# Kernel optimization log

Hardware: AMD Instinct MI355X
Metric: run time of the kernel (lower is better)

Reference implementation:

```python
import jax, jax.numpy as jnp
import numpy as np

Z_LOSS_COEF = 0.001
TOP_K = 8


def setup_inputs() -> dict:
    key = jax.random.key(0)
    ks = jax.random.split(key, 8)
    D, L, E, F, FS = 1024, 256, 64, 256, 1024  # d_model, latent, experts, latent d_ff, shared d_ff
    B, S = 1, 1024
    x = jax.random.normal(ks[0], (B, S, D), jnp.float32)
    gate_w = jax.random.normal(ks[1], (E, D), jnp.float32) * 0.01  # router, std=0.01 init
    expert_bias = jnp.zeros((E,), jnp.float32)  # load-balancing bias buffer
    down_w = jax.random.normal(ks[2], (L, D), jnp.float32) * 0.02
    up_w = jax.random.normal(ks[3], (D, L), jnp.float32) * 0.02
    shared_gu_w = jax.random.normal(ks[4], (2 * FS, D), jnp.float32) * 0.02
    shared_down_w = jax.random.normal(ks[5], (D, FS), jnp.float32) * 0.02
    exp_gu_w = jax.random.normal(ks[6], (E, L, 2 * F), jnp.float32) * 0.02  # [E,K,N] layout
    exp_down_w = jax.random.normal(ks[7], (E, F, L), jnp.float32) * 0.02
    return {"x": x, "gate_w": gate_w, "expert_bias": expert_bias,
            "down_w": down_w, "up_w": up_w,
            "shared_gu_w": shared_gu_w, "shared_down_w": shared_down_w,
            "exp_gu_w": exp_gu_w, "exp_down_w": exp_down_w}


def reference(x, gate_w, expert_bias, down_w, up_w, shared_gu_w, shared_down_w, exp_gu_w, exp_down_w):
    B, S, D = x.shape
    xf = x.reshape(-1, D)                     # [N, D]
    N = xf.shape[0]
    E = gate_w.shape[0]
    # ---- AuxLossFreeRouter (full d_model input) ----
    logits = xf @ gate_w.T                    # [N, E]
    z_loss = Z_LOSS_COEF * jnp.mean(jax.nn.logsumexp(logits, axis=-1) ** 2)
    affinity = jax.nn.sigmoid(logits)
    scores = affinity + expert_bias           # bias only affects selection, not weights
    _, sel = jax.lax.top_k(scores, TOP_K)     # [N, K] int32
    sel_aff = jnp.take_along_axis(affinity, sel, axis=1)
    gw = sel_aff / (sel_aff.sum(-1, keepdims=True) + 1e-9)  # [N, K]
    # sparse combine matrix [N, E]
    combine = jnp.zeros((N, E), xf.dtype).at[jnp.arange(N)[:, None], sel].add(gw)
    # ---- shared SwiGLU expert at full d_model ----
    sh = xf @ shared_gu_w.T
    g, u = jnp.split(sh, 2, axis=-1)
    shared_out = (jax.nn.silu(g) * u) @ shared_down_w.T     # [N, D]
    # ---- latent batched experts: down-project, dense-over-E SwiGLU, sparse combine ----
    lat = xf @ down_w.T                       # [N, L]
    h = jnp.einsum('nl,elf->nef', lat, exp_gu_w)            # [N, E, 2F]
    hg, hu = jnp.split(h, 2, axis=-1)
    hid = jax.nn.silu(hg) * hu                # [N, E, F]
    y = jnp.einsum('nef,efl->nel', hid, exp_down_w)         # [N, E, L]
    routed_lat = jnp.einsum('ne,nel->nl', combine, y)       # sparse top-k combine
    routed = routed_lat @ up_w.T              # [N, D]
    out = (shared_out + routed).reshape(B, S, D)
    return out, z_loss
```

## Files before the change

### kernel.cpp

```cpp
#include <hip/hip_runtime.h>
#include <stdint.h>


using f32x4 = __attribute__((ext_vector_type(4))) float;
using s16x8 = __attribute__((ext_vector_type(8))) short;

#define MFMA_BF16(a, b, c) __builtin_amdgcn_mfma_f32_16x16x32_bf16((a), (b), (c), 0, 0, 0)
#define AS1 __attribute__((address_space(1)))
#define AS3 __attribute__((address_space(3)))

__device__ __forceinline__ unsigned short f2bf(float f) {
  union { float f; uint32_t u; } v; v.f = f;
  uint32_t u = v.u;
  u += 0x7FFFu + ((u >> 16) & 1u);
  return (unsigned short)(u >> 16);
}
__device__ __forceinline__ float bf2f(unsigned short h) {
  union { uint32_t u; float f; } v; v.u = ((uint32_t)h) << 16;
  return v.f;
}
__device__ __forceinline__ float silu_f(float x) { return x / (1.f + expf(-x)); }

__device__ __forceinline__ size_t TIDX(int row, int col, int K) {
  return (((size_t)((row >> 7) * (K >> 5) + (col >> 5))) << 12) +
         (size_t)((((col >> 3) & 3) << 10) + ((row & 127) << 3) + (col & 7));
}

struct Args {
  const float *x, *gate, *down, *sgu, *sdw, *up, *egu, *edw, *bias;
  unsigned short *xb, *Wcat, *Bf, *egut, *edwt, *Abuf, *lat_g, *hide, *ybuf;
  float *C1, *Pf, *out;
  int *counts, *slot_nk;
  float *gw_nk;
};

__global__ void pack_kernel(Args a) {
  __shared__ union { float lin[128 * 33]; float tp[32][33]; } sm;
  const int b = blockIdx.x, t = threadIdx.x;
  if (b == 0) {
    if (t < 64) a.counts[t] = 0;
    if (t == 64) a.out[1048576] = 0.f;
  }
  if (b < 1184) {
    int rt, kt, K;
    const float* base = nullptr;
    unsigned short* dst;
    if (b < 608)      { rt = b >> 5;          kt = b & 31; K = 1024; dst = a.Wcat; }
    else if (b < 928) { int q = b - 608; rt = q / 40; kt = q % 40; K = 1280; dst = a.Bf; }
    else              { int q = b - 928; rt = q >> 5; kt = q & 31; K = 1024; dst = a.xb; base = a.x; }

    const int r = t >> 1, half = t & 1;
    const int gr = rt * 128 + r;
    const int c0 = kt * 32 + half * 16;
    const float* s;
    if (b < 608) {
      if (gr < 64)       s = a.gate + (size_t)gr * 1024 + c0;
      else if (gr < 320) s = a.down + (size_t)(gr - 64) * 1024 + c0;
      else if (gr < 384) s = nullptr;
      else {
        const int i = gr - 384;
        s = a.sgu + (size_t)((i >> 1) + (i & 1) * 1024) * 1024 + c0;
      }
    } else if (b < 928) {
      s = (c0 < 1024) ? a.sdw + (size_t)gr * 1024 + c0
                      : a.up + (size_t)gr * 256 + (c0 - 1024);
    } else {
      s = base + (size_t)gr * 1024 + c0;
    }
#pragma unroll
    for (int i = 0; i < 4; ++i) {
      float4 v = s ? *(const float4*)(s + i * 4) : make_float4(0.f, 0.f, 0.f, 0.f);
      sm.lin[r * 33 + half * 16 + i * 4 + 0] = v.x;
      sm.lin[r * 33 + half * 16 + i * 4 + 1] = v.y;
      sm.lin[r * 33 + half * 16 + i * 4 + 2] = v.z;
      sm.lin[r * 33 + half * 16 + i * 4 + 3] = v.w;
    }
    __syncthreads();
    const int j = t >> 6, r0 = (t & 63) * 2;
    unsigned short tmp[16];
#pragma unroll
    for (int rr = 0; rr < 2; ++rr)
#pragma unroll
      for (int c = 0; c < 8; ++c)
        tmp[rr * 8 + c] = f2bf(sm.lin[(r0 + rr) * 33 + j * 8 + c]);
    unsigned short* d = dst + ((size_t)(rt * (K >> 5) + kt) << 12) + t * 16;
    *(s16x8*)d = *(s16x8*)tmp;
    *(s16x8*)(d + 8) = *(s16x8*)(tmp + 8);
  } else {
    const float* src; unsigned short* dst; int lds, tr, tc; bool inter;
    if (b < 9376) {
      const int q = b - 1184, e = q >> 7, tt = q & 127;
      tr = tt >> 4; tc = tt & 15; lds = 512; inter = true;
      src = a.egu + (size_t)e * 131072; dst = a.egut + (size_t)e * 131072;
    } else {
      const int q = b - 9376, e = q >> 6, tt = q & 63;
      tr = tt >> 3; tc = tt & 7; lds = 256; inter = false;
      src = a.edw + (size_t)e * 65536; dst = a.edwt + (size_t)e * 65536;
    }
    const int r = t >> 3, c4 = (t & 7) * 4;
    float4 v = *(const float4*)(src + (size_t)(tr * 32 + r) * lds + tc * 32 + c4);
    sm.tp[r][c4 + 0] = v.x; sm.tp[r][c4 + 1] = v.y;
    sm.tp[r][c4 + 2] = v.z; sm.tp[r][c4 + 3] = v.w;
    __syncthreads();
    const int n = tc * 32 + r;
    const int orow = inter ? ((n < 256) ? 2 * n : 2 * (n - 256) + 1) : n;
    const int col = tr * 32 + c4;
    ushort4 o = make_ushort4(f2bf(sm.tp[c4 + 0][r]), f2bf(sm.tp[c4 + 1][r]),
                             f2bf(sm.tp[c4 + 2][r]), f2bf(sm.tp[c4 + 3][r]));
    *(ushort4*)(dst + TIDX(orow, col, 256)) = o;
  }
}

template <int MODE>
__device__ void wgemm64(const unsigned short* __restrict__ A, int KA, int m0,
                        const unsigned short* __restrict__ B, int KB, int n0,
                        int kt0, int nkt, void* __restrict__ out, int ld, int coff,
                        unsigned short* __restrict__ L) {
  const int lane = threadIdx.x & 63;
  const unsigned short* Abase =
      A + (((size_t)((m0 >> 7) * (KA >> 5) + kt0)) << 12) + ((m0 >> 6) & 1) * 512;
  const unsigned short* Bbase =
      B + (((size_t)((n0 >> 7) * (KB >> 5) + kt0)) << 12) + ((n0 >> 6) & 1) * 512;
  unsigned short* As = L;
  unsigned short* Bs = L + 4096;

  auto stage = [&](int kt, int buf) {
    const unsigned short* at = Abase + ((size_t)kt << 12);
    const unsigned short* bt = Bbase + ((size_t)kt << 12);
#pragma unroll
    for (int j = 0; j < 4; ++j)
      __builtin_amdgcn_global_load_lds((const AS1 void*)(at + j * 1024 + lane * 8),
                                       (AS3 void*)(As + buf * 2048 + j * 512), 16, 0, 0);
#pragma unroll
    for (int j = 0; j < 4; ++j)
      __builtin_amdgcn_global_load_lds((const AS1 void*)(bt + j * 1024 + lane * 8),
                                       (AS3 void*)(Bs + buf * 2048 + j * 512), 16, 0, 0);
  };

  f32x4 acc[4][4] = {};
  stage(0, 0);
  const int kh = lane >> 4, r16 = lane & 15;
  for (int kt = 0; kt < nkt; ++kt) {
    if (kt + 1 < nkt) {
      stage(kt + 1, (kt + 1) & 1);
      asm volatile("s_waitcnt vmcnt(8)" ::: "memory");
    } else {
      asm volatile("s_waitcnt vmcnt(0)" ::: "memory");
    }
    const unsigned short* Ac = As + (kt & 1) * 2048;
    const unsigned short* Bc = Bs + (kt & 1) * 2048;
    s16x8 af[4], bfr[4];
#pragma unroll
    for (int m = 0; m < 4; ++m)
      af[m] = *(const s16x8*)(Ac + kh * 512 + (m * 16 + r16) * 8);
#pragma unroll
    for (int n = 0; n < 4; ++n)
      bfr[n] = *(const s16x8*)(Bc + kh * 512 + (n * 16 + r16) * 8);
#pragma unroll
    for (int m = 0; m < 4; ++m)
#pragma unroll
      for (int n = 0; n < 4; ++n)
        acc[m][n] = MFMA_BF16(af[m], bfr[n], acc[m][n]);
  }

#pragma unroll
  for (int m = 0; m < 4; ++m) {
    const int rb = m0 + m * 16 + (lane >> 4) * 4;
#pragma unroll
    for (int n = 0; n < 4; ++n) {
      const int c = n0 + n * 16 + (lane & 15);
      if (MODE == 0) {
        float* O = (float*)out;
#pragma unroll
        for (int j = 0; j < 4; ++j) O[(size_t)(rb + j) * ld + c] = acc[m][n][j];
      } else if (MODE == 1) {
        unsigned short* O = (unsigned short*)out;
#pragma unroll
        for (int j = 0; j < 4; ++j) O[TIDX(rb + j, c, ld)] = f2bf(acc[m][n][j]);
      } else {
        unsigned short* O = (unsigned short*)out;
        const int col = (c - coff) >> 1;
#pragma unroll
        for (int j = 0; j < 4; ++j) {
          const float v = acc[m][n][j];
          const float u = __shfl_xor(v, 1);
          if (!(lane & 1)) O[TIDX(rb + j, col, ld)] = f2bf(silu_f(v) * u);
        }
      }
    }
  }
}

__global__ __launch_bounds__(64, 3) void wg1(const unsigned short* __restrict__ xb,
                                             const unsigned short* __restrict__ Wcat,
                                             float* __restrict__ C1,
                                             unsigned short* __restrict__ Abuf) {
  __shared__ __align__(16) unsigned short L[8192];
  const int b = blockIdx.x, mt = b / 38, nt = b % 38;
  if (nt < 6)
    wgemm64<0>(xb, 1024, mt * 64, Wcat, 1024, nt * 64, 0, 32, C1, 384, 0, L);
  else
    wgemm64<2>(xb, 1024, mt * 64, Wcat, 1024, nt * 64, 0, 32, Abuf, 1280, 384, L);
}

__global__ __launch_bounds__(64, 3) void wgGU(const unsigned short* __restrict__ lat_g,
                                              const unsigned short* __restrict__ egut,
                                              unsigned short* __restrict__ hide,
                                              const int* __restrict__ counts) {
  __shared__ __align__(16) unsigned short L[8192];
  const int b = blockIdx.x, e = b >> 5, rt = (b >> 3) & 3, ct = b & 7;
  int cnt = counts[e];
  if (cnt > 256) cnt = 256;
  if (rt * 64 >= cnt) return;
  wgemm64<2>(lat_g, 256, e * 256 + rt * 64, egut + (size_t)e * 131072, 256,
             ct * 64, 0, 8, hide, 256, 0, L);
}

__global__ __launch_bounds__(64, 3) void wgDW(const unsigned short* __restrict__ hide,
                                              const unsigned short* __restrict__ edwt,
                                              unsigned short* __restrict__ ybuf,
                                              const int* __restrict__ counts) {
  __shared__ __align__(16) unsigned short L[8192];
  const int b = blockIdx.x, e = b >> 4, rt = (b >> 2) & 3, ct = b & 3;
  int cnt = counts[e];
  if (cnt > 256) cnt = 256;
  if (rt * 64 >= cnt) return;
  wgemm64<1>(hide, 256, e * 256 + rt * 64, edwt + (size_t)e * 65536, 256,
             ct * 64, 0, 8, ybuf, 256, 0, L);
}

__global__ __launch_bounds__(64, 3) void wgF(const unsigned short* __restrict__ Abuf,
                                             const unsigned short* __restrict__ Bf,
                                             float* __restrict__ Pf) {
  __shared__ __align__(16) unsigned short L[8192];
  const int b = blockIdx.x, kc = b >> 8, mt = (b >> 4) & 15, nt = b & 15;
  wgemm64<0>(Abuf, 1280, mt * 64, Bf, 1280, nt * 64, kc * 10, 10,
             Pf + (size_t)kc * 1048576, 1024, 0, L);
}

__global__ void addF(const float* __restrict__ Pf, float* __restrict__ out) {
  const size_t i = (size_t)blockIdx.x * 1024 + threadIdx.x * 4;
  float4 s = *(const float4*)(Pf + i);
  const float4 b1 = *(const float4*)(Pf + 1048576 + i);
  const float4 b2 = *(const float4*)(Pf + 2097152 + i);
  const float4 b3 = *(const float4*)(Pf + 3145728 + i);
  s.x += b1.x + b2.x + b3.x; s.y += b1.y + b2.y + b3.y;
  s.z += b1.z + b2.z + b3.z; s.w += b1.w + b2.w + b3.w;
  *(float4*)(out + i) = s;
}

__global__ void router_kernel(Args a) {
  const int n = blockIdx.x * 4 + (threadIdx.x >> 6);
  const int lane = threadIdx.x & 63;
  const float* row = a.C1 + (size_t)n * 384;
  const float logit = row[lane];

  float mx = logit;
#pragma unroll
  for (int d = 32; d; d >>= 1) mx = fmaxf(mx, __shfl_xor(mx, d));
  float se = expf(logit - mx);
#pragma unroll
  for (int d = 32; d; d >>= 1) se += __shfl_xor(se, d);
  if (lane == 0) {
    const float lse = mx + logf(se);
    atomicAdd(a.out + 1048576, 0.001f * lse * lse * (1.f / 1024.f));
  }

  const float aff = 1.f / (1.f + expf(-logit));
  float s = aff + a.bias[lane];

  float asum = 0.f;
  int e_mine = 0; float a_mine = 0.f;
#pragma unroll
  for (int k = 0; k < 8; ++k) {
    float m2 = s;
#pragma unroll
    for (int d = 32; d; d >>= 1) m2 = fmaxf(m2, __shfl_xor(m2, d));
    const unsigned long long blt = __ballot(s == m2);
    const int idx = __ffsll(blt) - 1;
    const float af_ = __shfl(aff, idx);
    asum += af_;
    if (lane == k) { e_mine = idx; a_mine = af_; }
    if (lane == idx) s = -3.0e38f;
  }
  const float inv = 1.f / (asum + 1e-9f);

  int slot = 0;
  if (lane < 8) {
    int pos = atomicAdd(&a.counts[e_mine], 1);
    if (pos > 255) pos = 255;
    slot = e_mine * 256 + pos;
    a.slot_nk[(size_t)n * 8 + lane] = slot;
    a.gw_nk[(size_t)n * 8 + lane] = a_mine * inv;
  }

  const float4 lv = *(const float4*)(row + 64 + lane * 4);
  const ushort4 lb = make_ushort4(f2bf(lv.x), f2bf(lv.y), f2bf(lv.z), f2bf(lv.w));
#pragma unroll
  for (int k = 0; k < 8; ++k) {
    const int sl = __shfl(slot, k);
    *(ushort4*)(a.lat_g + TIDX(sl, lane * 4, 256)) = lb;
  }
}

__global__ void combine_kernel(Args a) {
  const int n = blockIdx.x * 4 + (threadIdx.x >> 6);
  const int l4 = (threadIdx.x & 63) * 4;
  float a0 = 0.f, a1 = 0.f, a2 = 0.f, a3 = 0.f;
#pragma unroll
  for (int k = 0; k < 8; ++k) {
    const int sl = a.slot_nk[(size_t)n * 8 + k];
    const float g = a.gw_nk[(size_t)n * 8 + k];
    const ushort4 yv = *(const ushort4*)(a.ybuf + TIDX(sl, l4, 256));
    a0 += g * bf2f(yv.x); a1 += g * bf2f(yv.y);
    a2 += g * bf2f(yv.z); a3 += g * bf2f(yv.w);
  }
  *(ushort4*)(a.Abuf + TIDX(n, 1024 + l4, 1280)) =
      make_ushort4(f2bf(a0), f2bf(a1), f2bf(a2), f2bf(a3));
}

extern "C" void kernel_launch(void* const* d_in, const int* in_sizes, int n_in,
                              void* d_out, int out_size, void* d_ws, size_t ws_size,
                              hipStream_t stream) {
  (void)in_sizes; (void)n_in; (void)out_size; (void)ws_size;
  Args a;
  a.x    = (const float*)d_in[0];
  a.gate = (const float*)d_in[1];
  a.bias = (const float*)d_in[2];
  a.down = (const float*)d_in[3];
  a.up   = (const float*)d_in[4];
  a.sgu  = (const float*)d_in[5];
  a.sdw  = (const float*)d_in[6];
  a.egu  = (const float*)d_in[7];
  a.edw  = (const float*)d_in[8];
  a.out  = (float*)d_out;

  char* w = (char*)d_ws;
  auto alloc = [&](size_t bytes) { char* p = w; w += (bytes + 255) & ~(size_t)255; return p; };
  a.xb    = (unsigned short*)alloc(1048576ull * 2);
  a.Wcat  = (unsigned short*)alloc(2432ull * 1024 * 2);
  a.Bf    = (unsigned short*)alloc(1024ull * 1280 * 2);
  a.egut  = (unsigned short*)alloc(64ull * 512 * 256 * 2);
  a.edwt  = (unsigned short*)alloc(64ull * 256 * 256 * 2);
  a.C1    = (float*)alloc(1024ull * 384 * 4);
  a.Abuf  = (unsigned short*)alloc(1024ull * 1280 * 2);
  a.lat_g = (unsigned short*)alloc(16384ull * 256 * 2);
  a.hide  = (unsigned short*)alloc(16384ull * 256 * 2);
  a.ybuf  = (unsigned short*)alloc(16384ull * 256 * 2);
  a.Pf    = (float*)alloc(4ull * 1048576 * 4);
  a.counts  = (int*)alloc(64 * 4);
  a.slot_nk = (int*)alloc(8192 * 4);
  a.gw_nk   = (float*)alloc(8192 * 4);

  pack_kernel<<<dim3(13472), dim3(256), 0, stream>>>(a);
  wg1<<<dim3(608), dim3(64), 0, stream>>>(a.xb, a.Wcat, a.C1, a.Abuf);
  router_kernel<<<dim3(256), dim3(256), 0, stream>>>(a);
  wgGU<<<dim3(2048), dim3(64), 0, stream>>>(a.lat_g, a.egut, a.hide, a.counts);
  wgDW<<<dim3(1024), dim3(64), 0, stream>>>(a.hide, a.edwt, a.ybuf, a.counts);
  combine_kernel<<<dim3(256), dim3(256), 0, stream>>>(a);
  wgF<<<dim3(1024), dim3(64), 0, stream>>>(a.Abuf, a.Bf, a.Pf);
  addF<<<dim3(1024), dim3(256), 0, stream>>>(a.Pf, a.out);
}
```

Measured before the change: 126.6 us.

## Load GEMM fragments directly from global into registers, dropping LDS staging

The single-wave 64x64 GEMM tile no longer stages A and B through LDS with global_load_lds. Each lane now loads its MFMA fragments straight from the pre-tiled global layout into registers, double-buffered two k-steps ahead. This removes the LDS round trip and the shared-memory allocation, which may raise occupancy. In exchange it uses more registers and relies on the tiled layout giving coalesced 16-byte loads, with latency hidden only by the register prefetch.

```diff
diff --git a/kernel.cpp b/kernel.cpp
--- a/kernel.cpp
+++ b/kernel.cpp
@@ -6,8 +6,6 @@
 using s16x8 = __attribute__((ext_vector_type(8))) short;
 
 #define MFMA_BF16(a, b, c) __builtin_amdgcn_mfma_f32_16x16x32_bf16((a), (b), (c), 0, 0, 0)
-#define AS1 __attribute__((address_space(1)))
-#define AS3 __attribute__((address_space(3)))
 
 __device__ __forceinline__ unsigned short f2bf(float f) {
   union { float f; uint32_t u; } v; v.f = f;
@@ -114,53 +112,44 @@
 template <int MODE>
 __device__ void wgemm64(const unsigned short* __restrict__ A, int KA, int m0,
                         const unsigned short* __restrict__ B, int KB, int n0,
-                        int kt0, int nkt, void* __restrict__ out, int ld, int coff,
-                        unsigned short* __restrict__ L) {
+                        int kt0, int nkt, void* __restrict__ out, int ld, int coff) {
   const int lane = threadIdx.x & 63;
-  const unsigned short* Abase =
-      A + (((size_t)((m0 >> 7) * (KA >> 5) + kt0)) << 12) + ((m0 >> 6) & 1) * 512;
-  const unsigned short* Bbase =
-      B + (((size_t)((n0 >> 7) * (KB >> 5) + kt0)) << 12) + ((n0 >> 6) & 1) * 512;
-  unsigned short* As = L;
-  unsigned short* Bs = L + 4096;
-
-  auto stage = [&](int kt, int buf) {
-    const unsigned short* at = Abase + ((size_t)kt << 12);
-    const unsigned short* bt = Bbase + ((size_t)kt << 12);
-#pragma unroll
-    for (int j = 0; j < 4; ++j)
-      __builtin_amdgcn_global_load_lds((const AS1 void*)(at + j * 1024 + lane * 8),
-                                       (AS3 void*)(As + buf * 2048 + j * 512), 16, 0, 0);
-#pragma unroll
-    for (int j = 0; j < 4; ++j)
-      __builtin_amdgcn_global_load_lds((const AS1 void*)(bt + j * 1024 + lane * 8),
-                                       (AS3 void*)(Bs + buf * 2048 + j * 512), 16, 0, 0);
+  const int kh = lane >> 4, r16 = lane & 15;
+  const unsigned short* pa =
+      A + (((size_t)((m0 >> 7) * (KA >> 5) + kt0)) << 12) + ((m0 >> 6) & 1) * 512 +
+      kh * 1024 + r16 * 8;
+  const unsigned short* pb =
+      B + (((size_t)((n0 >> 7) * (KB >> 5) + kt0)) << 12) + ((n0 >> 6) & 1) * 512 +
+      kh * 1024 + r16 * 8;
+
+  s16x8 A0[4], B0[4], A1[4], B1[4];
+
+  auto LD = [&](s16x8* Sa, s16x8* Sb, int kt) {
+    const unsigned short* qa = pa + ((size_t)kt << 12);
+    const unsigned short* qb = pb + ((size_t)kt << 12);
+#pragma unroll
+    for (int m = 0; m < 4; ++m) Sa[m] = *(const s16x8*)(qa + m * 128);
+#pragma unroll
+    for (int n = 0; n < 4; ++n) Sb[n] = *(const s16x8*)(qb + n * 128);
   };
 
   f32x4 acc[4][4] = {};
-  stage(0, 0);
-  const int kh = lane >> 4, r16 = lane & 15;
-  for (int kt = 0; kt < nkt; ++kt) {
-    if (kt + 1 < nkt) {
-      stage(kt + 1, (kt + 1) & 1);
-      asm volatile("s_waitcnt vmcnt(8)" ::: "memory");
-    } else {
-      asm volatile("s_waitcnt vmcnt(0)" ::: "memory");
-    }
-    const unsigned short* Ac = As + (kt & 1) * 2048;
-    const unsigned short* Bc = Bs + (kt & 1) * 2048;
-    s16x8 af[4], bfr[4];
+  LD(A0, B0, 0);
+  if (nkt > 1) LD(A1, B1, 1);
+
+  for (int kt = 0; kt < nkt; kt += 2) {
 #pragma unroll
     for (int m = 0; m < 4; ++m)
-      af[m] = *(const s16x8*)(Ac + kh * 512 + (m * 16 + r16) * 8);
-#pragma unroll
-    for (int n = 0; n < 4; ++n)
-      bfr[n] = *(const s16x8*)(Bc + kh * 512 + (n * 16 + r16) * 8);
+#pragma unroll
+      for (int n = 0; n < 4; ++n)
+        acc[m][n] = MFMA_BF16(A0[m], B0[n], acc[m][n]);
+    if (kt + 2 < nkt) LD(A0, B0, kt + 2);
 #pragma unroll
     for (int m = 0; m < 4; ++m)
 #pragma unroll
       for (int n = 0; n < 4; ++n)
-        acc[m][n] = MFMA_BF16(af[m], bfr[n], acc[m][n]);
+        acc[m][n] = MFMA_BF16(A1[m], B1[n], acc[m][n]);
+    if (kt + 3 < nkt) LD(A1, B1, kt + 3);
   }
 
 #pragma unroll
@@ -195,47 +184,43 @@
                                              const unsigned short* __restrict__ Wcat,
                                              float* __restrict__ C1,
                                              unsigned short* __restrict__ Abuf) {
-  __shared__ __align__(16) unsigned short L[8192];
   const int b = blockIdx.x, mt = b / 38, nt = b % 38;
   if (nt < 6)
-    wgemm64<0>(xb, 1024, mt * 64, Wcat, 1024, nt * 64, 0, 32, C1, 384, 0, L);
+    wgemm64<0>(xb, 1024, mt * 64, Wcat, 1024, nt * 64, 0, 32, C1, 384, 0);
   else
-    wgemm64<2>(xb, 1024, mt * 64, Wcat, 1024, nt * 64, 0, 32, Abuf, 1280, 384, L);
+    wgemm64<2>(xb, 1024, mt * 64, Wcat, 1024, nt * 64, 0, 32, Abuf, 1280, 384);
 }
 
 __global__ __launch_bounds__(64, 3) void wgGU(const unsigned short* __restrict__ lat_g,
                                               const unsigned short* __restrict__ egut,
                                               unsigned short* __restrict__ hide,
                                               const int* __restrict__ counts) {
-  __shared__ __align__(16) unsigned short L[8192];
   const int b = blockIdx.x, e = b >> 5, rt = (b >> 3) & 3, ct = b & 7;
   int cnt = counts[e];
   if (cnt > 256) cnt = 256;
   if (rt * 64 >= cnt) return;
   wgemm64<2>(lat_g, 256, e * 256 + rt * 64, egut + (size_t)e * 131072, 256,
-             ct * 64, 0, 8, hide, 256, 0, L);
+             ct * 64, 0, 8, hide, 256, 0);
 }
 
 __global__ __launch_bounds__(64, 3) void wgDW(const unsigned short* __restrict__ hide,
                                               const unsigned short* __restrict__ edwt,
                                               unsigned short* __restrict__ ybuf,
                                               const int* __restrict__ counts) {
-  __shared__ __align__(16) unsigned short L[8192];
   const int b = blockIdx.x, e = b >> 4, rt = (b >> 2) & 3, ct = b & 3;
   int cnt = counts[e];
   if (cnt > 256) cnt = 256;
   if (rt * 64 >= cnt) return;
   wgemm64<1>(hide, 256, e * 256 + rt * 64, edwt + (size_t)e * 65536, 256,
-             ct * 64, 0, 8, ybuf, 256, 0, L);
+             ct * 64, 0, 8, ybuf, 256, 0);
 }
 
 __global__ __launch_bounds__(64, 3) void wgF(const unsigned short* __restrict__ Abuf,
                                              const unsigned short* __restrict__ Bf,
                                              float* __restrict__ Pf) {
-  __shared__ __align__(16) unsigned short L[8192];
   const int b = blockIdx.x, kc = b >> 8, mt = (b >> 4) & 15, nt = b & 15;
   wgemm64<0>(Abuf, 1280, mt * 64, Bf, 1280, nt * 64, kc * 10, 10,
-             Pf + (size_t)kc * 1048576, 1024, 0, L);
+             Pf + (size_t)kc * 1048576, 1024, 0);
 }
 
 __global__ void addF(const float* __restrict__ Pf, float* __restrict__ out) {
```

After: 130.7 us. +3.2%, slower.
